# Optimization experiments

Hardware: AMD Instinct MI355X
Metric: run time of the kernel (lower is better)

The kernel has to match this reference:

```python
import jax, jax.numpy as jnp
import numpy as np

W_GRID, H_GRID = 5, 5
N_NODES = W_GRID * H_GRID  # 25
N_NEI = 8
N_CLS = 10
BN_EPS = 1e-5


def _neighbors(i, w, h):
    """Replicates Brain.neighbors ordering exactly; pads missing slots with -1
    (the torch code pads with p1 == zeros at the END of the list)."""
    size = w * h
    n = []
    if i - w >= 0:
        n.append(i - w)
    if i % w != 0:
        n.append(i - 1)
    if (i + 1) % w != 0:
        n.append(i + 1)
    if i + w < size:
        n.append(i + w)
    if i - w - 1 >= 0 and i % w != 0:
        n.append(i - w - 1)
    if i - w + 1 >= 0 and (i + 1) % w != 0:
        n.append(i - w + 1)
    if i + w - 1 < size and i % w != 0:
        n.append(i + w - 1)
    if i + w + 1 < size and (i + 1) % w != 0:
        n.append(i + w + 1)
    while len(n) < N_NEI:
        n.append(-1)
    return n

NEI = np.array([_neighbors(i, W_GRID, H_GRID) for i in range(N_NODES)], dtype=np.int32)  # [25, 8]
NEI_CLIP = np.maximum(NEI, 0)
NEI_MASK = (NEI >= 0)


def conv_bn_relu(x, W, b, g, be, m, v):
    # Conv2d(k=3, s=1, p=1) + eval-mode BatchNorm2d + ReLU, NCHW layout
    y = jax.lax.conv_general_dilated(
        x, W, window_strides=(1, 1), padding=[(1, 1), (1, 1)],
        dimension_numbers=("NCHW", "OIHW", "NCHW"))
    y = y + b[None, :, None, None]
    scale = g / jnp.sqrt(v + BN_EPS)
    y = (y - m[None, :, None, None]) * scale[None, :, None, None] + be[None, :, None, None]
    return jax.nn.relu(y)


def maxpool3s2p1(x):
    # MaxPool2d(kernel=3, stride=2, padding=1)
    return jax.lax.reduce_window(
        x, -jnp.inf, jax.lax.max,
        window_dimensions=(1, 1, 3, 3), window_strides=(1, 1, 2, 2),
        padding=[(0, 0), (0, 0), (1, 1), (1, 1)])


def per_node_mlp(inp, Wa, ba, Wb, bb):
    # inp: [25, B, 336]; distinct Linear(336,600)-Tanh-Linear(600,10)-Softmax per node
    h = jnp.tanh(jnp.einsum("nbi,nih->nbh", inp, Wa) + ba[:, None, :])
    logits = jnp.einsum("nbh,nhc->nbc", h, Wb) + bb[:, None, :]
    return jax.nn.softmax(logits, axis=-1)  # [25, B, 10]


def setup_inputs() -> dict:
    key = jax.random.key(0)
    ks = iter(jax.random.split(key, 64))
    B, C = 8192, 3
    d = {"x": jax.random.normal(next(ks), (B, C, 20, 20), jnp.float32)}
    chans = [(C, 64), (64, 128), (128, 256), (256, 256)]
    for li, (ci, co) in enumerate(chans, start=1):
        d[f"W{li}"] = jax.random.normal(next(ks), (co, ci, 3, 3), jnp.float32) * 0.05
        d[f"b{li}"] = jax.random.normal(next(ks), (co,), jnp.float32) * 0.05
        d[f"g{li}"] = jax.random.uniform(next(ks), (co,), jnp.float32, 0.5, 1.5)
        d[f"be{li}"] = jax.random.normal(next(ks), (co,), jnp.float32) * 0.1
        d[f"m{li}"] = jax.random.normal(next(ks), (co,), jnp.float32) * 0.1
        d[f"v{li}"] = jax.random.uniform(next(ks), (co,), jnp.float32, 0.5, 1.5)
    d["Wa"] = jax.random.normal(next(ks), (N_NODES, 336, 600), jnp.float32) * 0.05
    d["ba"] = jax.random.normal(next(ks), (N_NODES, 600), jnp.float32) * 0.05
    d["Wb"] = jax.random.normal(next(ks), (N_NODES, 600, N_CLS), jnp.float32) * 0.05
    d["bb"] = jax.random.normal(next(ks), (N_NODES, N_CLS), jnp.float32) * 0.05
    return d


def reference(x, W1, b1, g1, be1, m1, v1, W2, b2, g2, be2, m2, v2,
              W3, b3, g3, be3, m3, v3, W4, b4, g4, be4, m4, v4,
              Wa, ba, Wb, bb):
    c = conv_bn_relu(x, W1, b1, g1, be1, m1, v1)
    c = maxpool3s2p1(c)                      # [B, 64, 10, 10]
    c = conv_bn_relu(c, W2, b2, g2, be2, m2, v2)
    c = maxpool3s2p1(c)                      # [B, 128, 5, 5]
    c = conv_bn_relu(c, W3, b3, g3, be3, m3, v3)
    c = conv_bn_relu(c, W4, b4, g4, be4, m4, v4)  # [B, 256, 5, 5]
    B = x.shape[0]
    feats = c.reshape(B, 256, N_NODES).transpose(2, 0, 1)  # [25, B, 256]
    # Stage 1: neighbor slots are all zeros (p1..p8 = zeros)
    zeros80 = jnp.zeros((N_NODES, B, N_NEI * N_CLS), x.dtype)
    preds = per_node_mlp(jnp.concatenate([zeros80, feats], axis=-1), Wa, ba, Wb, bb)  # [25, B, 10]
    # Stage 2: gather up to 8 neighbor predictions (ordered), pad missing with zeros
    nb = preds[jnp.asarray(NEI_CLIP)]                          # [25, 8, B, 10]
    nb = jnp.where(jnp.asarray(NEI_MASK)[:, :, None, None], nb, 0.0)
    nb = nb.transpose(0, 2, 1, 3).reshape(N_NODES, B, N_NEI * N_CLS)  # [25, B, 80]
    second = per_node_mlp(jnp.concatenate([nb, feats], axis=-1), Wa, ba, Wb, bb)  # [25, B, 10]
    mean_predictions = second.mean(axis=0)  # [B, 10]
    return mean_predictions, second
```

## Files before the change

kernel.cpp:

```cpp
#include <hip/hip_runtime.h>

typedef unsigned short u16;
typedef unsigned int u32;

typedef __attribute__((ext_vector_type(8))) __bf16 bf16x8;
typedef __attribute__((ext_vector_type(4))) float f32x4;

__device__ __forceinline__ float bf2f(u16 u) {
    u32 t = ((u32)u) << 16;
    float f;
    __builtin_memcpy(&f, &t, 4);
    return f;
}
__device__ __forceinline__ u16 f2bf(float f) {
    u32 u;
    __builtin_memcpy(&u, &f, 4);
    u32 r = (u + 0x7fffu + ((u >> 16) & 1u)) >> 16;
    return (u16)r;
}
__device__ __forceinline__ float tanh_fast(float x) {
    float xc = fminf(fmaxf(x, -15.f), 15.f);
    float e = __expf(2.f * xc);
    return (e - 1.f) / (e + 1.f);
}

__device__ __forceinline__ void gld16(const u16* g, u16* l) {
    __builtin_amdgcn_global_load_lds(
        (const __attribute__((address_space(1))) u32*)(uintptr_t)g,
        (__attribute__((address_space(3))) u32*)(u32)(uintptr_t)l,
        16, 0, 0);
}


template <int EPI, int NT>
__global__ __launch_bounds__(256, 3) void gemm_bt(
    const u16* __restrict__ A, const u16* __restrict__ W, u16* __restrict__ O,
    const float* __restrict__ epiA, const float* __restrict__ epiB,
    int Kin, int N, int T, int Himg, int Wimg,
    int ldA, int ldW, int ldO,
    long long Az, long long Wz, long long Oz, int epiZ,
    int Bc, int bshift)
{
    constexpr int NJ = NT / 32;
    __shared__ __align__(16) u16 lsA[2][128 * 32];
    __shared__ __align__(16) u16 lsW[2][NT * 32];

    const int tid = threadIdx.x;
    const int z = blockIdx.z;
    A += (long long)z * Az;
    W += (long long)z * Wz;
    O += (long long)z * Oz;
    epiB += (long long)z * epiZ;

    const int m0 = blockIdx.x * 128;
    const int n0 = blockIdx.y * NT;
    const int s = m0 >> bshift;
    const int b0 = m0 & (Bc - 1);
    const int hh0 = s / Wimg, ww0 = s % Wimg;

    const int wave = tid >> 6;
    const int lane = tid & 63;
    const int mbase = (wave >> 1) * 64;
    const int nbase = (wave & 1) * (NT / 2);
    const int ln = lane & 15, qd = lane >> 4;

    const int srow = lane >> 2;
    const int sc = (((lane & 3) - ((srow >> 1) & 3)) & 3) * 8;
    const int csel = ((qd + (ln >> 1)) & 3) * 8;

    const int rowA = wave * 32 + srow;
    const int rowW = (NT == 128) ? (wave * 32 + srow) : (wave * 16 + srow);
    const int offA0 = rowA * ldA + sc;
    const int offA1 = offA0 + 16 * ldA;
    const int offW0 = rowW * ldW + sc;
    const int offW1 = offW0 + 16 * ldW;
    u16* const lA0 = &lsA[0][0] + wave * 1024;
    u16* const lW0 = (NT == 128) ? (&lsW[0][0] + wave * 1024) : (&lsW[0][0] + wave * 512);
    constexpr int LPAR_A = 128 * 32;
    constexpr int LPAR_W = NT * 32;

    auto tapvalid = [&](int t) -> bool {
        if (T != 9) return true;
        const int hh = hh0 + t / 3 - 1, ww = ww0 + t % 3 - 1;
        return hh >= 0 && hh < Himg && ww >= 0 && ww < Wimg;
    };
    auto tapA = [&](int t) -> const u16* {
        int sp = s;
        if (T == 9) sp = (hh0 + t / 3 - 1) * Wimg + (ww0 + t % 3 - 1);
        return A + (long long)(sp * Bc + b0) * ldA;
    };

    int t0 = 0;
    while (!tapvalid(t0)) ++t0;
    int nvalid = 0;
    for (int t = 0; t < T; ++t) nvalid += tapvalid(t) ? 1 : 0;
    const int KS = Kin >> 5;
    const int S = nvalid * KS;

    const u16* Ab = tapA(t0);
    const u16* Wb = W + ((long long)t0 * N + n0) * ldW;

    gld16(Ab + offA0, lA0);
    gld16(Ab + offA1, lA0 + 512);
    gld16(Wb + offW0, lW0);
    if (NT == 128) gld16(Wb + offW1, lW0 + 512);

    int ntap = t0, nkk = 0;

    f32x4 acc[4][NJ];
#pragma unroll
    for (int i = 0; i < 4; ++i)
#pragma unroll
        for (int j = 0; j < NJ; ++j)
            acc[i][j] = (f32x4){0.f, 0.f, 0.f, 0.f};

    for (int st = 0; st < S; ++st) {
        __syncthreads();
        if (st + 1 < S) {
            nkk += 32;
            if (nkk == Kin) {
                nkk = 0;
                do { ++ntap; } while (!tapvalid(ntap));
                Ab = tapA(ntap);
                Wb = W + ((long long)ntap * N + n0) * ldW;
            }
            const int pp = (st + 1) & 1;
            gld16(Ab + offA0 + nkk, lA0 + pp * LPAR_A);
            gld16(Ab + offA1 + nkk, lA0 + pp * LPAR_A + 512);
            gld16(Wb + offW0 + nkk, lW0 + pp * LPAR_W);
            if (NT == 128) gld16(Wb + offW1 + nkk, lW0 + pp * LPAR_W + 512);
        }
        const int cp = st & 1;
        bf16x8 af[4], bfr[NJ];
#pragma unroll
        for (int f = 0; f < 4; ++f)
            af[f] = *(const bf16x8*)&lsA[cp][(mbase + f * 16 + ln) * 32 + csel];
#pragma unroll
        for (int f = 0; f < NJ; ++f)
            bfr[f] = *(const bf16x8*)&lsW[cp][(nbase + f * 16 + ln) * 32 + csel];
#pragma unroll
        for (int i = 0; i < 4; ++i)
#pragma unroll
            for (int j = 0; j < NJ; ++j)
                acc[i][j] = __builtin_amdgcn_mfma_f32_16x16x32_bf16(
                    af[i], bfr[j], acc[i][j], 0, 0, 0);
    }

#pragma unroll
    for (int j = 0; j < NJ; ++j) {
        const int n = n0 + nbase + j * 16 + ln;
        const float sh = epiB[n];
        float sc2 = 1.f;
        if (EPI == 0) sc2 = epiA[n];
#pragma unroll
        for (int i = 0; i < 4; ++i) {
            const int mrow = mbase + i * 16 + qd * 4;
#pragma unroll
            for (int rr = 0; rr < 4; ++rr) {
                float v = acc[i][j][rr];
                if (EPI == 0) v = fmaxf(v * sc2 + sh, 0.f);
                else          v = tanh_fast(v + sh);
                O[(long long)(m0 + mrow + rr) * ldO + n] = f2bf(v);
            }
        }
    }
}

__global__ __launch_bounds__(256) void conv1pool(
    const u16* __restrict__ xcol, const u16* __restrict__ W1t, u16* __restrict__ p1,
    const float* __restrict__ epiA, const float* __restrict__ epiB, int Bc)
{
    const int tid = threadIdx.x;
    const int wave = tid >> 6;
    const int lane = tid & 63;
    const int ln = lane & 15, qd = lane >> 4;

    const int b0 = blockIdx.x * 128;
    const int so = blockIdx.y;
    const int ho = so / 10, wo = so % 10;

    const int mbase = (wave >> 1) * 64;
    const int nbase = (wave & 1) * 32;

    bf16x8 bfr[2];
#pragma unroll
    for (int j = 0; j < 2; ++j)
        bfr[j] = *(const bf16x8*)&W1t[(nbase + j * 16 + ln) * 32 + qd * 8];

    float sc2[2], sh[2];
#pragma unroll
    for (int j = 0; j < 2; ++j) {
        const int n = nbase + j * 16 + ln;
        sc2[j] = epiA[n];
        sh[j] = epiB[n];
    }

    f32x4 best[4][2];
#pragma unroll
    for (int i = 0; i < 4; ++i)
#pragma unroll
        for (int j = 0; j < 2; ++j)
            best[i][j] = (f32x4){0.f, 0.f, 0.f, 0.f};

#pragma unroll
    for (int st = 0; st < 9; ++st) {
        int hh = 2 * ho - 1 + st / 3;
        int ww = 2 * wo - 1 + st % 3;
        hh = hh < 0 ? 0 : (hh > 19 ? 19 : hh);
        ww = ww < 0 ? 0 : (ww > 19 ? 19 : ww);
        const u16* Ab = xcol + (long long)((hh * 20 + ww) * Bc + b0) * 32;

        bf16x8 af[4];
#pragma unroll
        for (int f = 0; f < 4; ++f)
            af[f] = *(const bf16x8*)&Ab[(mbase + f * 16 + ln) * 32 + qd * 8];

#pragma unroll
        for (int i = 0; i < 4; ++i)
#pragma unroll
            for (int j = 0; j < 2; ++j) {
                f32x4 acc = (f32x4){0.f, 0.f, 0.f, 0.f};
                acc = __builtin_amdgcn_mfma_f32_16x16x32_bf16(af[i], bfr[j], acc, 0, 0, 0);
#pragma unroll
                for (int rr = 0; rr < 4; ++rr) {
                    const float v = fmaxf(acc[rr] * sc2[j] + sh[j], 0.f);
                    best[i][j][rr] = fmaxf(best[i][j][rr], v);
                }
            }
    }

#pragma unroll
    for (int j = 0; j < 2; ++j) {
        const int n = nbase + j * 16 + ln;
#pragma unroll
        for (int i = 0; i < 4; ++i) {
            const int mrow = mbase + i * 16 + qd * 4;
#pragma unroll
            for (int rr = 0; rr < 4; ++rr)
                p1[(long long)(so * Bc + b0 + mrow + rr) * 64 + n] = f2bf(best[i][j][rr]);
        }
    }
}

template <int STAGE>
__global__ __launch_bounds__(256) void logits_mfma(
    const u16* __restrict__ h, const u16* __restrict__ Wbp, const float* __restrict__ bbp,
    u16* __restrict__ preds, float* __restrict__ dout, int Bc, int gbase)
{
    __shared__ __align__(16) u16 lsA[2][128 * 32];
    __shared__ __align__(16) u16 lsW[2][16 * 32];

    const int tid = threadIdx.x;
    const int n = blockIdx.y;
    const int m0 = blockIdx.x * 128;
    const u16* A = h + ((long long)n * Bc + m0) * 640;
    const u16* Wn = Wbp + n * 16 * 640;

    const int wave = tid >> 6;
    const int lane = tid & 63;
    const int ln = lane & 15, qd = lane >> 4;
    const int srow = lane >> 2;
    const int sc = (((lane & 3) - ((srow >> 1) & 3)) & 3) * 8;
    const int csel = ((qd + (ln >> 1)) & 3) * 8;

    const int offA0 = (wave * 32 + srow) * 640 + sc;
    const int offA1 = offA0 + 16 * 640;
    const int offW0 = srow * 640 + sc;
    u16* const lA0 = &lsA[0][0] + wave * 1024;

    gld16(A + offA0, lA0);
    gld16(A + offA1, lA0 + 512);
    if (wave == 0) gld16(Wn + offW0, &lsW[0][0]);

    f32x4 acc[2];
    acc[0] = (f32x4){0.f, 0.f, 0.f, 0.f};
    acc[1] = (f32x4){0.f, 0.f, 0.f, 0.f};

    for (int st = 0; st < 20; ++st) {
        __syncthreads();
        if (st + 1 < 20) {
            const int kk = (st + 1) * 32;
            const int pp = (st + 1) & 1;
            gld16(A + offA0 + kk, lA0 + pp * 4096);
            gld16(A + offA1 + kk, lA0 + pp * 4096 + 512);
            if (wave == 0) gld16(Wn + offW0 + kk, &lsW[pp][0]);
        }
        const int cp = st & 1;
        const bf16x8 bfr = *(const bf16x8*)&lsW[cp][ln * 32 + csel];
        const bf16x8 a0 = *(const bf16x8*)&lsA[cp][(wave * 32 + ln) * 32 + csel];
        const bf16x8 a1 = *(const bf16x8*)&lsA[cp][(wave * 32 + 16 + ln) * 32 + csel];
        acc[0] = __builtin_amdgcn_mfma_f32_16x16x32_bf16(a0, bfr, acc[0], 0, 0, 0);
        acc[1] = __builtin_amdgcn_mfma_f32_16x16x32_bf16(a1, bfr, acc[1], 0, 0, 0);
    }

    const float bias = bbp[n * 16 + ln];
#pragma unroll
    for (int i = 0; i < 2; ++i) {
#pragma unroll
        for (int rr = 0; rr < 4; ++rr) {
            const float v = acc[i][rr] + bias;
            float mx = v;
#pragma unroll
            for (int mk = 1; mk < 16; mk <<= 1)
                mx = fmaxf(mx, __shfl_xor(mx, mk));
            const float e = __expf(v - mx);
            float ssum = e;
#pragma unroll
            for (int mk = 1; mk < 16; mk <<= 1)
                ssum += __shfl_xor(ssum, mk);
            const float p = e / ssum;
            const int row = m0 + wave * 32 + i * 16 + qd * 4 + rr;
            if (ln < 10) {
                if (STAGE == 1)
                    preds[((long long)n * Bc + row) * 10 + ln] = f2bf(p);
                else
                    dout[81920 + ((long long)n * 8192 + gbase + row) * 10 + ln] = p;
            }
        }
    }
}

__global__ __launch_bounds__(256) void transpose_x(
    const float* __restrict__ x, u16* __restrict__ xt, int Bc, int bshift)
{
    const int t = blockIdx.x * 256 + threadIdx.x;
    if (t >= 400 * Bc) return;
    const int s = t >> bshift;
    const int b = t & (Bc - 1);
    const u32 c0 = f2bf(x[((long long)b * 3 + 0) * 400 + s]);
    const u32 c1 = f2bf(x[((long long)b * 3 + 1) * 400 + s]);
    const u32 c2 = f2bf(x[((long long)b * 3 + 2) * 400 + s]);
    uint2 st;
    st.x = c0 | (c1 << 16);
    st.y = c2;
    *(uint2*)(xt + ((long long)s * Bc + b) * 4) = st;
}

__global__ __launch_bounds__(256) void im2col1(
    const u16* __restrict__ xt, u16* __restrict__ xcol, int Bc, int bshift)
{
    const int t = blockIdx.x * 256 + threadIdx.x;
    if (t >= 400 * Bc) return;
    const int s = t >> bshift;
    const int b = t & (Bc - 1);
    const int hh = s / 20, ww = s % 20;

    u32 p0, q0, p1, q1, p2, q2, p3, q3, p4, q4, p5, q5, p6, q6, p7, q7, p8, q8;
#define LOADTAP(T, P, Q)                                                      \
    {                                                                         \
        const int ih = hh + (T) / 3 - 1, iw = ww + (T) % 3 - 1;               \
        P = 0u; Q = 0u;                                                       \
        if (ih >= 0 && ih < 20 && iw >= 0 && iw < 20) {                       \
            const uint2 v = *(const uint2*)(xt +                              \
                ((long long)(ih * 20 + iw) * Bc + b) * 4);                    \
            P = v.x; Q = v.y;                                                 \
        }                                                                     \
    }
    LOADTAP(0, p0, q0) LOADTAP(1, p1, q1) LOADTAP(2, p2, q2)
    LOADTAP(3, p3, q3) LOADTAP(4, p4, q4) LOADTAP(5, p5, q5)
    LOADTAP(6, p6, q6) LOADTAP(7, p7, q7) LOADTAP(8, p8, q8)
#undef LOADTAP

    u16* o = xcol + (long long)t * 32;
    uint4 w;
    w.x = p0;                w.y = q0 | (p1 << 16);
    w.z = (p1 >> 16) | (q1 << 16);
    w.w = p2;
    *(uint4*)(o + 0) = w;
    w.x = q2 | (p3 << 16);   w.y = (p3 >> 16) | (q3 << 16);
    w.z = p4;                w.w = q4 | (p5 << 16);
    *(uint4*)(o + 8) = w;
    w.x = (p5 >> 16) | (q5 << 16);
    w.y = p6;                w.z = q6 | (p7 << 16);
    w.w = (p7 >> 16) | (q7 << 16);
    *(uint4*)(o + 16) = w;
    w.x = p8;                w.y = q8;
    w.z = 0u;                w.w = 0u;
    *(uint4*)(o + 24) = w;
}

template <int CH>
__global__ __launch_bounds__(256) void pool_k(
    const u16* __restrict__ src, u16* __restrict__ dst, int Bc, int Hi, int Ho)
{
    constexpr int G = CH / 8;
    const int t = blockIdx.x * 256 + threadIdx.x;
    const int cc = t & (G - 1);
    const int b = t / G;
    if (b >= Bc) return;
    const int so = blockIdx.y;
    const int ho = so / Ho, wo = so % Ho;
    float best[8];
#pragma unroll
    for (int e = 0; e < 8; ++e) best[e] = 0.f;
    for (int ph = 0; ph < 3; ++ph) {
        const int hh = 2 * ho - 1 + ph;
        if (hh < 0 || hh >= Hi) continue;
        for (int pw = 0; pw < 3; ++pw) {
            const int ww = 2 * wo - 1 + pw;
            if (ww < 0 || ww >= Hi) continue;
            const uint4 u = *(const uint4*)(src + ((long long)(hh * Hi + ww) * Bc + b) * CH + cc * 8);
            const u32 uw[4] = {u.x, u.y, u.z, u.w};
#pragma unroll
            for (int e = 0; e < 4; ++e) {
                best[2 * e]     = fmaxf(best[2 * e],     bf2f((u16)(uw[e] & 0xffff)));
                best[2 * e + 1] = fmaxf(best[2 * e + 1], bf2f((u16)(uw[e] >> 16)));
            }
        }
    }
    u32 pk[4];
#pragma unroll
    for (int e = 0; e < 4; ++e)
        pk[e] = (u32)f2bf(best[2 * e]) | (((u32)f2bf(best[2 * e + 1])) << 16);
    uint4 st;
    st.x = pk[0]; st.y = pk[1]; st.z = pk[2]; st.w = pk[3];
    *(uint4*)(dst + ((long long)so * Bc + b) * CH + cc * 8) = st;
}

__device__ __forceinline__ void neighbors5x5(int i, int* nb) {
    const int w = 5, size = 25;
    int cnt = 0;
    if (i - w >= 0) nb[cnt++] = i - w;
    if (i % w != 0) nb[cnt++] = i - 1;
    if ((i + 1) % w != 0) nb[cnt++] = i + 1;
    if (i + w < size) nb[cnt++] = i + w;
    if (i - w - 1 >= 0 && i % w != 0) nb[cnt++] = i - w - 1;
    if (i - w + 1 >= 0 && (i + 1) % w != 0) nb[cnt++] = i - w + 1;
    if (i + w - 1 < size && i % w != 0) nb[cnt++] = i + w - 1;
    if (i + w + 1 < size && (i + 1) % w != 0) nb[cnt++] = i + w + 1;
    for (; cnt < 8; ++cnt) nb[cnt] = -1;
}

__global__ __launch_bounds__(256) void gather_nb(
    const u16* __restrict__ preds, const u16* __restrict__ feats, u16* __restrict__ A2,
    int Bc, int bshift)
{
    const int g = blockIdx.x * 256 + threadIdx.x;
    if (g >= 25 * Bc) return;
    const int n = g >> bshift;
    const int b = g & (Bc - 1);
    int nb[8];
    neighbors5x5(n, nb);
    u16* dst = A2 + (long long)g * 352;
#pragma unroll
    for (int j = 0; j < 8; ++j) {
        u32* d32 = (u32*)(dst + j * 10);
        if (nb[j] >= 0) {
            const u32* s32 = (const u32*)(preds + ((long long)nb[j] * Bc + b) * 10);
#pragma unroll
            for (int q = 0; q < 5; ++q) d32[q] = s32[q];
        } else {
#pragma unroll
            for (int q = 0; q < 5; ++q) d32[q] = 0u;
        }
    }
    const uint4* fs = (const uint4*)(feats + (long long)g * 256);
    uint4* fd = (uint4*)(dst + 80);
#pragma unroll
    for (int q = 0; q < 32; ++q) fd[q] = fs[q];
    uint4 z;
    z.x = 0u; z.y = 0u; z.z = 0u; z.w = 0u;
    *(uint4*)(dst + 336) = z;
    *(uint4*)(dst + 344) = z;
}

__global__ __launch_bounds__(256) void mean_k(float* __restrict__ dout)
{
    const int t = blockIdx.x * 256 + threadIdx.x;
    float s = 0.f;
#pragma unroll
    for (int n = 0; n < 25; ++n) s += dout[81920 + n * 81920 + t];
    dout[t] = s * 0.04f;
}

__global__ void prep_bn_all(
    const float* b1, const float* g1, const float* be1, const float* m1, const float* v1,
    const float* b2, const float* g2, const float* be2, const float* m2, const float* v2,
    const float* b3, const float* g3, const float* be3, const float* m3, const float* v3,
    const float* b4, const float* g4, const float* be4, const float* m4, const float* v4,
    float* bnA, float* bnB)
{
    const int t = blockIdx.x * 256 + threadIdx.x;
    if (t >= 704) return;
    const float *bp, *gp, *bep, *mp, *vp;
    int idx;
    if (t < 64)       { bp=b1; gp=g1; bep=be1; mp=m1; vp=v1; idx=t; }
    else if (t < 192) { bp=b2; gp=g2; bep=be2; mp=m2; vp=v2; idx=t-64; }
    else if (t < 448) { bp=b3; gp=g3; bep=be3; mp=m3; vp=v3; idx=t-192; }
    else              { bp=b4; gp=g4; bep=be4; mp=m4; vp=v4; idx=t-448; }
    const float A = gp[idx] * rsqrtf(vp[idx] + 1e-5f);
    bnA[t] = A;
    bnB[t] = (bp[idx] - mp[idx]) * A + bep[idx];
}

__global__ void prep_w1col(const float* __restrict__ W1, u16* __restrict__ W1t)
{
    const int t = blockIdx.x * 256 + threadIdx.x;
    if (t >= 64 * 32) return;
    const int n = t >> 5, k = t & 31;
    u16 v = 0;
    if (k < 27) {
        const int tap = k / 3, ci = k % 3;
        v = f2bf(W1[n * 27 + ci * 9 + tap]);
    }
    W1t[t] = v;
}

__global__ void prep_convw(const float* __restrict__ W, u16* __restrict__ Wt, int Co, int Ci)
{
    const int t = blockIdx.x * 256 + threadIdx.x;
    const int tot = 9 * Co * Ci;
    if (t >= tot) return;
    const int sh = t / (Co * Ci);
    const int rem = t % (Co * Ci);
    const int co = rem / Ci, ci = rem % Ci;
    Wt[t] = f2bf(W[(long long)(co * Ci + ci) * 9 + sh]);
}

__global__ void prep_wat(const float* __restrict__ Wa, u16* __restrict__ Wat)
{
    const int t = blockIdx.x * 256 + threadIdx.x;
    if (t >= 25 * 640 * 352) return;
    const int n = t / (640 * 352);
    const int rem = t % (640 * 352);
    const int hcol = rem / 352;
    const int k = rem % 352;
    float v = 0.f;
    if (hcol < 600 && k < 336) v = Wa[((long long)n * 336 + k) * 600 + hcol];
    Wat[t] = f2bf(v);
}

__global__ void prep_ba(const float* __restrict__ ba, float* __restrict__ bap)
{
    const int t = blockIdx.x * 256 + threadIdx.x;
    if (t >= 25 * 640) return;
    const int n = t / 640, hcol = t % 640;
    bap[t] = (hcol < 600) ? ba[n * 600 + hcol] : 0.f;
}

__global__ void prep_wbt(const float* __restrict__ Wb, const float* __restrict__ bb,
                         u16* __restrict__ Wbp, float* __restrict__ bbp)
{
    const int t = blockIdx.x * 256 + threadIdx.x;
    if (t < 25 * 16 * 640) {
        const int n = t / (16 * 640);
        const int rem = t % (16 * 640);
        const int c = rem / 640, k = rem % 640;
        u16 v = 0;
        if (c < 10 && k < 600) v = f2bf(Wb[((long long)n * 600 + k) * 10 + c]);
        Wbp[t] = v;
    }
    if (t < 25 * 16) {
        const int n = t >> 4, c = t & 15;
        bbp[t] = (c < 10) ? bb[n * 10 + c] : -1e30f;
    }
}

extern "C" void kernel_launch(void* const* d_in, const int* in_sizes, int n_in,
                              void* d_out, int out_size, void* d_ws, size_t ws_size,
                              hipStream_t stream)
{
    (void)in_sizes; (void)n_in; (void)out_size;

    const float* x  = (const float*)d_in[0];
    const float* W1 = (const float*)d_in[1];
    const float* b1 = (const float*)d_in[2];
    const float* g1 = (const float*)d_in[3];
    const float* be1= (const float*)d_in[4];
    const float* m1 = (const float*)d_in[5];
    const float* v1 = (const float*)d_in[6];
    const float* W2 = (const float*)d_in[7];
    const float* b2 = (const float*)d_in[8];
    const float* g2 = (const float*)d_in[9];
    const float* be2= (const float*)d_in[10];
    const float* m2 = (const float*)d_in[11];
    const float* v2 = (const float*)d_in[12];
    const float* W3 = (const float*)d_in[13];
    const float* b3 = (const float*)d_in[14];
    const float* g3 = (const float*)d_in[15];
    const float* be3= (const float*)d_in[16];
    const float* m3 = (const float*)d_in[17];
    const float* v3 = (const float*)d_in[18];
    const float* W4 = (const float*)d_in[19];
    const float* b4 = (const float*)d_in[20];
    const float* g4 = (const float*)d_in[21];
    const float* be4= (const float*)d_in[22];
    const float* m4 = (const float*)d_in[23];
    const float* v4 = (const float*)d_in[24];
    const float* Wa = (const float*)d_in[25];
    const float* ba = (const float*)d_in[26];
    const float* Wb = (const float*)d_in[27];
    const float* bb = (const float*)d_in[28];
    float* dout = (float*)d_out;

    auto al = [](long long v) { return (v + 255LL) & ~255LL; };
    const long long fixedB = al(4096) + al(147456) + al(589824) + al(1179648) +
                             al(11264000) + al(64000) + al(2816) + al(2816) +
                             al(512000) + al(1600);
    int Bc = 256;
    for (int cand = 2048; cand >= 256; cand >>= 1) {
        long long need = fixedB + al(80000LL * cand);
        if (need <= (long long)ws_size) { Bc = cand; break; }
    }
    const int bshift = __builtin_ctz((unsigned)Bc);
    const int C = 8192 / Bc;

    char* wsp = (char*)d_ws;
    long long off = 0;
    auto alloc = [&](long long bytes) { long long o = off; off += al(bytes); return o; };
    u16* W1t  = (u16*)(wsp + alloc(4096));
    u16* Wt2  = (u16*)(wsp + alloc(147456));
    u16* Wt3  = (u16*)(wsp + alloc(589824));
    u16* Wt4  = (u16*)(wsp + alloc(1179648));
    u16* Wat  = (u16*)(wsp + alloc(11264000));
    float* bap = (float*)(wsp + alloc(64000));
    float* bnA = (float*)(wsp + alloc(2816));
    float* bnB = (float*)(wsp + alloc(2816));
    u16* Wbp  = (u16*)(wsp + alloc(512000));
    float* bbp = (float*)(wsp + alloc(1600));
    char* ch = wsp + alloc(80000LL * Bc);
    u16* xt   = (u16*)(ch + 0LL     * Bc);
    u16* xcol = (u16*)(ch + 3200LL  * Bc);
    u16* p1   = (u16*)(ch + 28800LL * Bc);
    u16* a2   = (u16*)(ch + 0LL     * Bc);
    u16* p2   = (u16*)(ch + 25600LL * Bc);
    u16* a3   = (u16*)(ch + 0LL     * Bc);
    u16* a4   = (u16*)(ch + 12800LL * Bc);
    u16* h1   = (u16*)(ch + 25600LL * Bc);
    u16* preds= (u16*)(ch + 57600LL * Bc);
    u16* A2   = (u16*)(ch + 25600LL * Bc);
    u16* h2   = (u16*)(ch + 43200LL * Bc);

    prep_bn_all<<<dim3(3), 256, 0, stream>>>(b1,g1,be1,m1,v1, b2,g2,be2,m2,v2,
                                             b3,g3,be3,m3,v3, b4,g4,be4,m4,v4, bnA, bnB);
    prep_w1col<<<dim3(8), 256, 0, stream>>>(W1, W1t);
    prep_convw<<<dim3(288),  256, 0, stream>>>(W2, Wt2, 128, 64);
    prep_convw<<<dim3(1152), 256, 0, stream>>>(W3, Wt3, 256, 128);
    prep_convw<<<dim3(2304), 256, 0, stream>>>(W4, Wt4, 256, 256);
    prep_wat<<<dim3(22000), 256, 0, stream>>>(Wa, Wat);
    prep_ba<<<dim3(63), 256, 0, stream>>>(ba, bap);
    prep_wbt<<<dim3(1000), 256, 0, stream>>>(Wb, bb, Wbp, bbp);

    for (int c = 0; c < C; ++c) {
        const float* xc = x + (long long)c * Bc * 1200;

        transpose_x<<<dim3(400 * Bc / 256), 256, 0, stream>>>(xc, xt, Bc, bshift);
        im2col1<<<dim3(400 * Bc / 256), 256, 0, stream>>>(xt, xcol, Bc, bshift);
        conv1pool<<<dim3(Bc / 128, 100), 256, 0, stream>>>(xcol, W1t, p1, bnA, bnB, Bc);

        gemm_bt<0,128><<<dim3(100 * Bc / 128, 1), 256, 0, stream>>>(p1, Wt2, a2, bnA + 64, bnB + 64,
            64, 128, 9, 10, 10, 64, 64, 128, 0LL, 0LL, 0LL, 0, Bc, bshift);
        pool_k<128><<<dim3(Bc * 16 / 256, 25), 256, 0, stream>>>(a2, p2, Bc, 10, 5);

        gemm_bt<0,128><<<dim3(25 * Bc / 128, 2), 256, 0, stream>>>(p2, Wt3, a3, bnA + 192, bnB + 192,
            128, 256, 9, 5, 5, 128, 128, 256, 0LL, 0LL, 0LL, 0, Bc, bshift);
        gemm_bt<0,128><<<dim3(25 * Bc / 128, 2), 256, 0, stream>>>(a3, Wt4, a4, bnA + 448, bnB + 448,
            256, 256, 9, 5, 5, 256, 256, 256, 0LL, 0LL, 0LL, 0, Bc, bshift);

        gemm_bt<1,128><<<dim3(Bc / 128, 5, 25), 256, 0, stream>>>(a4, Wat + 80, h1, nullptr, bap,
            256, 640, 1, 1, 1, 256, 352, 640,
            (long long)Bc * 256, 640LL * 352, (long long)Bc * 640, 640, Bc, bshift);
        logits_mfma<1><<<dim3(Bc / 128, 25), 256, 0, stream>>>(
            h1, Wbp, bbp, preds, nullptr, Bc, 0);

        gather_nb<<<dim3(25 * Bc / 256, 1), 256, 0, stream>>>(preds, a4, A2, Bc, bshift);
        gemm_bt<1,128><<<dim3(Bc / 128, 5, 25), 256, 0, stream>>>(A2, Wat, h2, nullptr, bap,
            352, 640, 1, 1, 1, 352, 352, 640,
            (long long)Bc * 352, 640LL * 352, (long long)Bc * 640, 640, Bc, bshift);
        logits_mfma<2><<<dim3(Bc / 128, 25), 256, 0, stream>>>(
            h2, Wbp, bbp, nullptr, dout, Bc, c * Bc);
    }

    mean_k<<<dim3(320), 256, 0, stream>>>(dout);
}
```

Baseline: 1.572 ms.

## Fuse per-node MLP hidden layer, tanh and logits/softmax into one kernel

```diff
diff --git a/kernel.cpp b/kernel.cpp
--- a/kernel.cpp
+++ b/kernel.cpp
@@ -21,7 +21,7 @@
 __device__ __forceinline__ float tanh_fast(float x) {
     float xc = fminf(fmaxf(x, -15.f), 15.f);
     float e = __expf(2.f * xc);
-    return (e - 1.f) / (e + 1.f);
+    return (e - 1.f) * __builtin_amdgcn_rcpf(e + 1.f);
 }
 
 __device__ __forceinline__ void gld16(const u16* g, u16* l) {
@@ -166,6 +166,160 @@
     }
 }
 
+template <int STAGE>
+__global__ __launch_bounds__(256, 2) void mlp_head(
+    const u16* __restrict__ A, const u16* __restrict__ W,
+    const float* __restrict__ bap, const u16* __restrict__ Wbp,
+    const float* __restrict__ bbp,
+    u16* __restrict__ preds, float* __restrict__ dout,
+    int Kin, int Bc, int gbase)
+{
+    __shared__ __align__(16) u16 lsA[2][128 * 32];
+    __shared__ __align__(16) u16 lsW[2][128 * 32];
+    __shared__ __align__(16) u16 lsH[128 * 132];
+
+    const int tid = threadIdx.x;
+    const int z = blockIdx.z;
+    A += (long long)z * Bc * Kin;
+    W += (long long)z * 640 * 352;
+    const float* bz = bap + z * 640;
+
+    const int m0 = blockIdx.x * 128;
+    const int wave = tid >> 6;
+    const int lane = tid & 63;
+    const int mbase = (wave >> 1) * 64;
+    const int nbase = (wave & 1) * 64;
+    const int ln = lane & 15, qd = lane >> 4;
+    const int srow = lane >> 2;
+    const int sc = (((lane & 3) - ((srow >> 1) & 3)) & 3) * 8;
+    const int csel = ((qd + (ln >> 1)) & 3) * 8;
+
+    const int rowS = wave * 32 + srow;
+    const int offA0 = rowS * Kin + sc;
+    const int offA1 = offA0 + 16 * Kin;
+    const int offW0 = rowS * 352 + sc;
+    const int offW1 = offW0 + 16 * 352;
+    u16* const lA0 = &lsA[0][0] + wave * 1024;
+    u16* const lW0 = &lsW[0][0] + wave * 1024;
+
+    const int KS = Kin >> 5;
+    const int Stot = 5 * KS;
+
+    const u16* Ab = A + (long long)m0 * Kin;
+    const u16* Wb = W;
+    int pnt = 0, pnkk = 0;
+
+    gld16(Ab + offA0, lA0);
+    gld16(Ab + offA1, lA0 + 512);
+    gld16(Wb + offW0, lW0);
+    gld16(Wb + offW1, lW0 + 512);
+
+    f32x4 acc[4][4];
+#pragma unroll
+    for (int i = 0; i < 4; ++i)
+#pragma unroll
+        for (int j = 0; j < 4; ++j)
+            acc[i][j] = (f32x4){0.f, 0.f, 0.f, 0.f};
+    f32x4 acc_lg[2];
+    acc_lg[0] = (f32x4){0.f, 0.f, 0.f, 0.f};
+    acc_lg[1] = (f32x4){0.f, 0.f, 0.f, 0.f};
+
+    int g = 0;
+    for (int nt = 0; nt < 5; ++nt) {
+        for (int st = 0; st < KS; ++st, ++g) {
+            __syncthreads();
+            if (g + 1 < Stot) {
+                pnkk += 32;
+                if (pnkk == Kin) {
+                    pnkk = 0;
+                    ++pnt;
+                    Wb = W + (long long)pnt * 128 * 352;
+                }
+                const int pp = (g + 1) & 1;
+                gld16(Ab + offA0 + pnkk, lA0 + pp * (128 * 32));
+                gld16(Ab + offA1 + pnkk, lA0 + pp * (128 * 32) + 512);
+                gld16(Wb + offW0 + pnkk, lW0 + pp * (128 * 32));
+                gld16(Wb + offW1 + pnkk, lW0 + pp * (128 * 32) + 512);
+            }
+            const int cp = g & 1;
+            bf16x8 af[4], bfr[4];
+#pragma unroll
+            for (int f = 0; f < 4; ++f)
+                af[f] = *(const bf16x8*)&lsA[cp][(mbase + f * 16 + ln) * 32 + csel];
+#pragma unroll
+            for (int f = 0; f < 4; ++f)
+                bfr[f] = *(const bf16x8*)&lsW[cp][(nbase + f * 16 + ln) * 32 + csel];
+#pragma unroll
+            for (int i = 0; i < 4; ++i)
+#pragma unroll
+                for (int j = 0; j < 4; ++j)
+                    acc[i][j] = __builtin_amdgcn_mfma_f32_16x16x32_bf16(
+                        af[i], bfr[j], acc[i][j], 0, 0, 0);
+        }
+
+#pragma unroll
+        for (int j = 0; j < 4; ++j) {
+            const int hc = nbase + j * 16 + ln;
+            const float sh = bz[nt * 128 + hc];
+#pragma unroll
+            for (int i = 0; i < 4; ++i) {
+                const int br = mbase + i * 16 + qd * 4;
+#pragma unroll
+                for (int rr = 0; rr < 4; ++rr)
+                    lsH[(br + rr) * 132 + hc] = f2bf(tanh_fast(acc[i][j][rr] + sh));
+                acc[i][j] = (f32x4){0.f, 0.f, 0.f, 0.f};
+            }
+        }
+        bf16x8 bfrg[4];
+#pragma unroll
+        for (int ks = 0; ks < 4; ++ks)
+            bfrg[ks] = *(const bf16x8*)&Wbp[((long long)z * 16 + ln) * 640 +
+                                            nt * 128 + ks * 32 + qd * 8];
+        __syncthreads();
+
+#pragma unroll
+        for (int ks = 0; ks < 4; ++ks) {
+#pragma unroll
+            for (int i = 0; i < 2; ++i) {
+                const int base = (wave * 32 + i * 16 + ln) * 132 + ks * 32 + qd * 8;
+                const uint2 u0 = *(const uint2*)&lsH[base];
+                const uint2 u1 = *(const uint2*)&lsH[base + 4];
+                u32 w4[4] = {u0.x, u0.y, u1.x, u1.y};
+                bf16x8 a8;
+                __builtin_memcpy(&a8, w4, 16);
+                acc_lg[i] = __builtin_amdgcn_mfma_f32_16x16x32_bf16(
+                    a8, bfrg[ks], acc_lg[i], 0, 0, 0);
+            }
+        }
+    }
+
+    const float bias = bbp[z * 16 + ln];
+#pragma unroll
+    for (int i = 0; i < 2; ++i) {
+#pragma unroll
+        for (int rr = 0; rr < 4; ++rr) {
+            const float v = acc_lg[i][rr] + bias;
+            float mx = v;
+#pragma unroll
+            for (int mk = 1; mk < 16; mk <<= 1)
+                mx = fmaxf(mx, __shfl_xor(mx, mk));
+            const float e = __expf(v - mx);
+            float ssum = e;
+#pragma unroll
+            for (int mk = 1; mk < 16; mk <<= 1)
+                ssum += __shfl_xor(ssum, mk);
+            const float p = e / ssum;
+            const int row = m0 + wave * 32 + i * 16 + qd * 4 + rr;
+            if (ln < 10) {
+                if (STAGE == 1)
+                    preds[((long long)z * Bc + row) * 10 + ln] = f2bf(p);
+                else
+                    dout[81920 + ((long long)z * 8192 + gbase + row) * 10 + ln] = p;
+            }
+        }
+    }
+}
+
 __global__ __launch_bounds__(256) void conv1pool(
     const u16* __restrict__ xcol, const u16* __restrict__ W1t, u16* __restrict__ p1,
     const float* __restrict__ epiA, const float* __restrict__ epiB, int Bc)
@@ -238,84 +392,6 @@
 #pragma unroll
             for (int rr = 0; rr < 4; ++rr)
                 p1[(long long)(so * Bc + b0 + mrow + rr) * 64 + n] = f2bf(best[i][j][rr]);
-        }
-    }
-}
-
-template <int STAGE>
-__global__ __launch_bounds__(256) void logits_mfma(
-    const u16* __restrict__ h, const u16* __restrict__ Wbp, const float* __restrict__ bbp,
-    u16* __restrict__ preds, float* __restrict__ dout, int Bc, int gbase)
-{
-    __shared__ __align__(16) u16 lsA[2][128 * 32];
-    __shared__ __align__(16) u16 lsW[2][16 * 32];
-
-    const int tid = threadIdx.x;
-    const int n = blockIdx.y;
-    const int m0 = blockIdx.x * 128;
-    const u16* A = h + ((long long)n * Bc + m0) * 640;
-    const u16* Wn = Wbp + n * 16 * 640;
-
-    const int wave = tid >> 6;
-    const int lane = tid & 63;
-    const int ln = lane & 15, qd = lane >> 4;
-    const int srow = lane >> 2;
-    const int sc = (((lane & 3) - ((srow >> 1) & 3)) & 3) * 8;
-    const int csel = ((qd + (ln >> 1)) & 3) * 8;
-
-    const int offA0 = (wave * 32 + srow) * 640 + sc;
-    const int offA1 = offA0 + 16 * 640;
-    const int offW0 = srow * 640 + sc;
-    u16* const lA0 = &lsA[0][0] + wave * 1024;
-
-    gld16(A + offA0, lA0);
-    gld16(A + offA1, lA0 + 512);
-    if (wave == 0) gld16(Wn + offW0, &lsW[0][0]);
-
-    f32x4 acc[2];
-    acc[0] = (f32x4){0.f, 0.f, 0.f, 0.f};
-    acc[1] = (f32x4){0.f, 0.f, 0.f, 0.f};
-
-    for (int st = 0; st < 20; ++st) {
-        __syncthreads();
-        if (st + 1 < 20) {
-            const int kk = (st + 1) * 32;
-            const int pp = (st + 1) & 1;
-            gld16(A + offA0 + kk, lA0 + pp * 4096);
-            gld16(A + offA1 + kk, lA0 + pp * 4096 + 512);
-            if (wave == 0) gld16(Wn + offW0 + kk, &lsW[pp][0]);
-        }
-        const int cp = st & 1;
-        const bf16x8 bfr = *(const bf16x8*)&lsW[cp][ln * 32 + csel];
-        const bf16x8 a0 = *(const bf16x8*)&lsA[cp][(wave * 32 + ln) * 32 + csel];
-        const bf16x8 a1 = *(const bf16x8*)&lsA[cp][(wave * 32 + 16 + ln) * 32 + csel];
-        acc[0] = __builtin_amdgcn_mfma_f32_16x16x32_bf16(a0, bfr, acc[0], 0, 0, 0);
-        acc[1] = __builtin_amdgcn_mfma_f32_16x16x32_bf16(a1, bfr, acc[1], 0, 0, 0);
-    }
-
-    const float bias = bbp[n * 16 + ln];
-#pragma unroll
-    for (int i = 0; i < 2; ++i) {
-#pragma unroll
-        for (int rr = 0; rr < 4; ++rr) {
-            const float v = acc[i][rr] + bias;
-            float mx = v;
-#pragma unroll
-            for (int mk = 1; mk < 16; mk <<= 1)
-                mx = fmaxf(mx, __shfl_xor(mx, mk));
-            const float e = __expf(v - mx);
-            float ssum = e;
-#pragma unroll
-            for (int mk = 1; mk < 16; mk <<= 1)
-                ssum += __shfl_xor(ssum, mk);
-            const float p = e / ssum;
-            const int row = m0 + wave * 32 + i * 16 + qd * 4 + rr;
-            if (ln < 10) {
-                if (STAGE == 1)
-                    preds[((long long)n * Bc + row) * 10 + ln] = f2bf(p);
-                else
-                    dout[81920 + ((long long)n * 8192 + gbase + row) * 10 + ln] = p;
-            }
         }
     }
 }
@@ -598,8 +674,8 @@
                              al(11264000) + al(64000) + al(2816) + al(2816) +
                              al(512000) + al(1600);
     int Bc = 256;
-    for (int cand = 2048; cand >= 256; cand >>= 1) {
-        long long need = fixedB + al(80000LL * cand);
+    for (int cand = 8192; cand >= 256; cand >>= 1) {
+        long long need = fixedB + al(44032LL * cand);
         if (need <= (long long)ws_size) { Bc = cand; break; }
     }
     const int bshift = __builtin_ctz((unsigned)Bc);
@@ -618,7 +694,7 @@
     float* bnB = (float*)(wsp + alloc(2816));
     u16* Wbp  = (u16*)(wsp + alloc(512000));
     float* bbp = (float*)(wsp + alloc(1600));
-    char* ch = wsp + alloc(80000LL * Bc);
+    char* ch = wsp + alloc(44032LL * Bc);
     u16* xt   = (u16*)(ch + 0LL     * Bc);
     u16* xcol = (u16*)(ch + 3200LL  * Bc);
     u16* p1   = (u16*)(ch + 28800LL * Bc);
@@ -626,10 +702,8 @@
     u16* p2   = (u16*)(ch + 25600LL * Bc);
     u16* a3   = (u16*)(ch + 0LL     * Bc);
     u16* a4   = (u16*)(ch + 12800LL * Bc);
-    u16* h1   = (u16*)(ch + 25600LL * Bc);
-    u16* preds= (u16*)(ch + 57600LL * Bc);
-    u16* A2   = (u16*)(ch + 25600LL * Bc);
-    u16* h2   = (u16*)(ch + 43200LL * Bc);
+    u16* preds= (u16*)(ch + 25600LL * Bc);
+    u16* A2   = (u16*)(ch + 26112LL * Bc);
 
     prep_bn_all<<<dim3(3), 256, 0, stream>>>(b1,g1,be1,m1,v1, b2,g2,be2,m2,v2,
                                              b3,g3,be3,m3,v3, b4,g4,be4,m4,v4, bnA, bnB);
@@ -657,18 +731,12 @@
         gemm_bt<0,128><<<dim3(25 * Bc / 128, 2), 256, 0, stream>>>(a3, Wt4, a4, bnA + 448, bnB + 448,
             256, 256, 9, 5, 5, 256, 256, 256, 0LL, 0LL, 0LL, 0, Bc, bshift);
 
-        gemm_bt<1,128><<<dim3(Bc / 128, 5, 25), 256, 0, stream>>>(a4, Wat + 80, h1, nullptr, bap,
-            256, 640, 1, 1, 1, 256, 352, 640,
-            (long long)Bc * 256, 640LL * 352, (long long)Bc * 640, 640, Bc, bshift);
-        logits_mfma<1><<<dim3(Bc / 128, 25), 256, 0, stream>>>(
-            h1, Wbp, bbp, preds, nullptr, Bc, 0);
+        mlp_head<1><<<dim3(Bc / 128, 1, 25), 256, 0, stream>>>(
+            a4, Wat + 80, bap, Wbp, bbp, preds, nullptr, 256, Bc, 0);
 
         gather_nb<<<dim3(25 * Bc / 256, 1), 256, 0, stream>>>(preds, a4, A2, Bc, bshift);
-        gemm_bt<1,128><<<dim3(Bc / 128, 5, 25), 256, 0, stream>>>(A2, Wat, h2, nullptr, bap,
-            352, 640, 1, 1, 1, 352, 352, 640,
-            (long long)Bc * 352, 640LL * 352, (long long)Bc * 640, 640, Bc, bshift);
-        logits_mfma<2><<<dim3(Bc / 128, 25), 256, 0, stream>>>(
-            h2, Wbp, bbp, nullptr, dout, Bc, c * Bc);
+        mlp_head<2><<<dim3(Bc / 128, 1, 25), 256, 0, stream>>>(
+            A2, Wat, bap, Wbp, bbp, nullptr, dout, 352, Bc, c * Bc);
     }
 
     mean_k<<<dim3(320), 256, 0, stream>>>(dout);
```

After: 1.398 ms. 1.12x faster.
